# Performance work log

Hardware: AMD Instinct MI355X
Metric: run time of the kernel (lower is better)

Reference implementation:

```python
import jax, jax.numpy as jnp
import numpy as np

B, S, H, DH = 64, 64, 64, 64  # S == H == DH required by the module's (buggy) shape logic
D = H * DH  # d_feature = 4096


def setup_inputs() -> dict:
    key = jax.random.key(0)
    ks = jax.random.split(key, 9)
    sc = 1.0 / np.sqrt(D).astype(np.float32)
    return {
        "x": jax.random.normal(ks[0], (B, S, D), jnp.float32),
        "Wq": jax.random.normal(ks[1], (D, D), jnp.float32) * sc,
        "bq": jax.random.normal(ks[2], (D,), jnp.float32) * 0.01,
        "Wk": jax.random.normal(ks[3], (D, D), jnp.float32) * sc,
        "bk": jax.random.normal(ks[4], (D,), jnp.float32) * 0.01,
        "Wv": jax.random.normal(ks[5], (D, D), jnp.float32) * sc,
        "bv": jax.random.normal(ks[6], (D,), jnp.float32) * 0.01,
        "Wp": jax.random.normal(ks[7], (D, D), jnp.float32) * sc,
        "bp": jax.random.normal(ks[8], (D,), jnp.float32) * 0.01,
    }


def reference(x, Wq, bq, Wk, bk, Wv, bv, Wp, bp):
    b, s, d = x.shape
    # nn.Linear: y = x @ W^T + b
    q = (x @ Wq.T + bq).reshape(b, s, H, DH)  # _split's permute(0,1,2,3) is identity
    k = (x @ Wk.T + bk).reshape(b, s, H, DH)
    v = (x @ Wv.T + bv).reshape(b, s, H, DH)
    # scores over HEAD axis (per token), shape (b, S, H, H); scale by sqrt(d_k)=sqrt(DH)
    scores = jnp.einsum("bshd,bsed->bshe", q, k) / np.sqrt(DH).astype(np.float32)
    attn = jax.nn.softmax(scores, axis=-1)
    # attn @ V^T : out[b,s,i,j] = sum_k attn[b,s,i,k] * v[b,s,j,k]  (needs H == DH)
    vals = jnp.einsum("bsik,bsjk->bsij", attn, v)  # (b, S, H, H)
    # _merge: permute(0,2,1,3) -> (b, H, S, H), view(b, H, S*H); S*H == d_feature
    merged = jnp.transpose(vals, (0, 2, 1, 3)).reshape(b, H, s * H)
    return merged @ Wp.T + bp  # (b, H, d_feature)
```

## Files before the change

### kernel.cpp

```cpp
#include <hip/hip_runtime.h>

typedef __attribute__((ext_vector_type(8))) __bf16 bf16x8;
typedef __attribute__((ext_vector_type(4))) float f32x4;

__device__ __forceinline__ float bf2f(unsigned short u) {
    union { unsigned u; float f; } c; c.u = ((unsigned)u) << 16; return c.f;
}
__device__ __forceinline__ unsigned short f2bf(float f) {
    union { float f; unsigned u; } c; c.f = f;
    unsigned r = c.u + 0x7fffu + ((c.u >> 16) & 1u);
    return (unsigned short)(r >> 16);
}

#define GLD_LDS16(g, l) \
    __builtin_amdgcn_global_load_lds( \
        (const __attribute__((address_space(1))) void*)(g), \
        (__attribute__((address_space(3))) void*)(l), 16, 0, 0)

__global__ void __launch_bounds__(256) cvt_f32_bf16(
    const float* __restrict__ s0, unsigned short* __restrict__ d0,
    const float* __restrict__ s1, unsigned short* __restrict__ d1,
    const float* __restrict__ s2, unsigned short* __restrict__ d2,
    const float* __restrict__ s3, unsigned short* __restrict__ d3,
    const float* __restrict__ s4, unsigned short* __restrict__ d4)
{
    const float* s; unsigned short* d;
    if (blockIdx.z == 0)      { s = s0; d = d0; }
    else if (blockIdx.z == 1) { s = s1; d = d1; }
    else if (blockIdx.z == 2) { s = s2; d = d2; }
    else if (blockIdx.z == 3) { s = s3; d = d3; }
    else                      { s = s4; d = d4; }
    const size_t N = (size_t)4096 * 4096;
    const size_t stride = (size_t)gridDim.x * 256 * 4;
    for (size_t i = ((size_t)blockIdx.x * 256 + threadIdx.x) * 4; i < N; i += stride) {
        float4 v = *(const float4*)(s + i);
        ushort4 o;
        o.x = f2bf(v.x); o.y = f2bf(v.y); o.z = f2bf(v.z); o.w = f2bf(v.w);
        *(ushort4*)(d + i) = o;
    }
}

template <bool OUTF32>
__global__ void __launch_bounds__(512, 2) gemm256(
    const unsigned short* __restrict__ A,
    const unsigned short* __restrict__ W0, const float* __restrict__ b0, void* __restrict__ C0,
    const unsigned short* __restrict__ W1, const float* __restrict__ b1, void* __restrict__ C1,
    const unsigned short* __restrict__ W2, const float* __restrict__ b2, void* __restrict__ C2)
{
    constexpr int K = 4096;
    constexpr int NT = 64;
    extern __shared__ char smem[];

    const unsigned short* W; const float* bias; void* C;
    if (blockIdx.z == 0)      { W = W0; bias = b0; C = C0; }
    else if (blockIdx.z == 1) { W = W1; bias = b1; C = C1; }
    else                      { W = W2; bias = b2; C = C2; }

    const int tid  = threadIdx.x;
    const int lane = tid & 63;
    const int wave = tid >> 6;
    const int wm = wave >> 2;
    const int wn = wave & 3;
    const int m0 = blockIdx.y * 256;
    const int n0 = blockIdx.x * 256;

    const int p = tid << 4;
    const int o = p ^ (((p >> 9) & 1) << 5);
    const int srow = ((o >> 11) << 4) | ((o >> 6) & 15);
    const int scol = (((o >> 10) & 1) << 5) | ((o & 63) >> 1);
    const unsigned short* pA = A + (size_t)(m0 + srow) * K + scol;
    const unsigned short* pB = W + (size_t)(n0 + srow) * K + scol;

    const int fl = lane & 15;
    const int qg = lane >> 4;
    int rdoff = (fl << 6) + (qg << 4);
    rdoff ^= (fl & 8) << 2;
    const int aOffc = (wm << 14) + rdoff;
    const int bOffc = 32768 + ((wn >> 1) << 14) + ((wn & 1) << 13) + rdoff;

    f32x4 acc[8][4];
#pragma unroll
    for (int i = 0; i < 8; i++)
#pragma unroll
        for (int j = 0; j < 4; j++) acc[i][j] = (f32x4){0.f, 0.f, 0.f, 0.f};

    bf16x8 af[4][2], bfr0[2][2], bfr1[2][2];

#define STAGE_A(tt, h, bb) do { \
    GLD_LDS16(pA + (size_t)(tt) * 64 + (size_t)(h) * 524288, \
              smem + (bb) * 65536 + (h) * 16384 + (wave << 10)); \
    GLD_LDS16(pA + (size_t)(tt) * 64 + (size_t)(h) * 524288 + 262144, \
              smem + (bb) * 65536 + (h) * 16384 + 8192 + (wave << 10)); \
} while (0)
#define STAGE_B(tt, h, bb) do { \
    GLD_LDS16(pB + (size_t)(tt) * 64 + (size_t)(h) * 524288, \
              smem + (bb) * 65536 + 32768 + (h) * 16384 + (wave << 10)); \
    GLD_LDS16(pB + (size_t)(tt) * 64 + (size_t)(h) * 524288 + 262144, \
              smem + (bb) * 65536 + 32768 + (h) * 16384 + 8192 + (wave << 10)); \
} while (0)

#define RD_A(mh, bb) do { \
    _Pragma("unroll") for (int it_ = 0; it_ < 4; ++it_) \
    _Pragma("unroll") for (int kk_ = 0; kk_ < 2; ++kk_) \
        af[it_][kk_] = *(const bf16x8*)(smem + (bb) * 65536 + aOffc + (mh) * 8192 + it_ * 2048 + kk_ * 1024); \
} while (0)
#define RD_B(nh, dst, bb) do { \
    _Pragma("unroll") for (int jt_ = 0; jt_ < 2; ++jt_) \
    _Pragma("unroll") for (int kk_ = 0; kk_ < 2; ++kk_) \
        dst[jt_][kk_] = *(const bf16x8*)(smem + (bb) * 65536 + bOffc + (nh) * 4096 + jt_ * 2048 + kk_ * 1024); \
} while (0)

#define MM(mh, nh, bset) do { \
    __builtin_amdgcn_s_setprio(1); \
    _Pragma("unroll") for (int it_ = 0; it_ < 4; ++it_) \
    _Pragma("unroll") for (int jt_ = 0; jt_ < 2; ++jt_) \
    _Pragma("unroll") for (int kk_ = 0; kk_ < 2; ++kk_) \
        acc[(mh) * 4 + it_][(nh) * 2 + jt_] = __builtin_amdgcn_mfma_f32_16x16x32_bf16( \
            af[it_][kk_], bset[jt_][kk_], acc[(mh) * 4 + it_][(nh) * 2 + jt_], 0, 0, 0); \
    __builtin_amdgcn_s_setprio(0); \
} while (0)

#define BAR() __builtin_amdgcn_s_barrier()
#define LGKM0 do { \
    asm volatile("s_waitcnt lgkmcnt(0)" ::: "memory"); \
    __builtin_amdgcn_sched_barrier(0); \
} while (0)

#define TILE(t, bb) do { \
    RD_A(0, bb); RD_B(0, bfr0, bb); \
    if ((t) + 1 < NT) STAGE_A((t) + 1, 0, (bb) ^ 1); \
    BAR(); LGKM0; MM(0, 0, bfr0); BAR(); \
    RD_B(1, bfr1, bb); \
    if ((t) + 1 < NT) STAGE_A((t) + 1, 1, (bb) ^ 1); \
    BAR(); LGKM0; MM(0, 1, bfr1); BAR(); \
    RD_A(1, bb); \
    if ((t) + 2 < NT) STAGE_B((t) + 2, 0, (bb)); \
    BAR(); LGKM0; MM(1, 0, bfr0); BAR(); \
    if ((t) + 2 < NT) STAGE_B((t) + 2, 1, (bb)); \
    BAR(); LGKM0; MM(1, 1, bfr1); \
    if ((t) + 2 < NT) { asm volatile("s_waitcnt vmcnt(4)" ::: "memory"); } \
    else              { asm volatile("s_waitcnt vmcnt(0)" ::: "memory"); } \
    BAR(); \
    __builtin_amdgcn_sched_barrier(0); \
} while (0)

    STAGE_A(0, 0, 0); STAGE_A(0, 1, 0);
    STAGE_B(0, 0, 0); STAGE_B(0, 1, 0);
    STAGE_B(1, 0, 1); STAGE_B(1, 1, 1);
    asm volatile("s_waitcnt vmcnt(4)" ::: "memory");
    BAR();
    __builtin_amdgcn_sched_barrier(0);

    for (int t = 0; t < NT; t += 2) {
        TILE(t, 0);
        TILE(t + 1, 1);
    }

    const int r0 = (lane >> 4) << 2;
#pragma unroll
    for (int j = 0; j < 4; ++j) {
        const int col = n0 + wn * 64 + j * 16 + fl;
        const float bj = bias[col];
#pragma unroll
        for (int i = 0; i < 8; ++i) {
            const int row = m0 + wm * 128 + i * 16 + r0;
#pragma unroll
            for (int r = 0; r < 4; ++r) {
                const float val = acc[i][j][r] + bj;
                if constexpr (OUTF32)
                    ((float*)C)[(size_t)(row + r) * 4096 + col] = val;
                else
                    ((unsigned short*)C)[(size_t)(row + r) * 4096 + col] = f2bf(val);
            }
        }
    }
#undef TILE
#undef LGKM0
#undef BAR
#undef MM
#undef RD_B
#undef RD_A
#undef STAGE_B
#undef STAGE_A
}

__global__ void __launch_bounds__(256) attn_mfma(
    const unsigned short* __restrict__ q, const unsigned short* __restrict__ k,
    const unsigned short* __restrict__ v, unsigned short* __restrict__ merged)
{
    __shared__ __align__(16) unsigned short sP[4][64 * 72];

    const int tid  = threadIdx.x;
    const int wave = tid >> 6;
    const int lane = tid & 63;
    const int token = blockIdx.x * 4 + wave;
    const int b = token >> 6, s = token & 63;
    const size_t base = (size_t)token * 4096;

    const int fl = lane & 15;
    const int qg = lane >> 4;

    f32x4 S[4][4];
#pragma unroll
    for (int i = 0; i < 4; i++)
#pragma unroll
        for (int j = 0; j < 4; j++) S[i][j] = (f32x4){0.f, 0.f, 0.f, 0.f};

#pragma unroll
    for (int ks = 0; ks < 2; ks++) {
        bf16x8 aq[4], bk[4];
#pragma unroll
        for (int t = 0; t < 4; t++) {
            aq[t] = *(const bf16x8*)(q + base + (size_t)(t * 16 + fl) * 64 + ks * 32 + qg * 8);
            bk[t] = *(const bf16x8*)(k + base + (size_t)(t * 16 + fl) * 64 + ks * 32 + qg * 8);
        }
#pragma unroll
        for (int i = 0; i < 4; i++)
#pragma unroll
            for (int j = 0; j < 4; j++)
                S[i][j] = __builtin_amdgcn_mfma_f32_16x16x32_bf16(aq[i], bk[j], S[i][j], 0, 0, 0);
    }

    float mrow[4][4];
#pragma unroll
    for (int i = 0; i < 4; i++)
#pragma unroll
        for (int r = 0; r < 4; r++) {
            float m = S[i][0][r];
            m = fmaxf(m, S[i][1][r]); m = fmaxf(m, S[i][2][r]); m = fmaxf(m, S[i][3][r]);
            mrow[i][r] = m;
        }
#pragma unroll
    for (int off = 1; off <= 8; off <<= 1)
#pragma unroll
        for (int i = 0; i < 4; i++)
#pragma unroll
            for (int r = 0; r < 4; r++)
                mrow[i][r] = fmaxf(mrow[i][r], __shfl_xor(mrow[i][r], off));

    float lrow[4][4];
#pragma unroll
    for (int i = 0; i < 4; i++)
#pragma unroll
        for (int r = 0; r < 4; r++) lrow[i][r] = 0.f;
#pragma unroll
    for (int i = 0; i < 4; i++)
#pragma unroll
        for (int j = 0; j < 4; j++)
#pragma unroll
            for (int r = 0; r < 4; r++) {
                const float p = __expf((S[i][j][r] - mrow[i][r]) * 0.125f);
                S[i][j][r] = p;
                lrow[i][r] += p;
            }
#pragma unroll
    for (int off = 1; off <= 8; off <<= 1)
#pragma unroll
        for (int i = 0; i < 4; i++)
#pragma unroll
            for (int r = 0; r < 4; r++)
                lrow[i][r] += __shfl_xor(lrow[i][r], off);

    unsigned short* myP = &sP[wave][0];
#pragma unroll
    for (int i = 0; i < 4; i++)
#pragma unroll
        for (int r = 0; r < 4; r++) {
            const float inv = 1.f / lrow[i][r];
            const int row = i * 16 + qg * 4 + r;
#pragma unroll
            for (int j = 0; j < 4; j++)
                myP[row * 72 + j * 16 + fl] = f2bf(S[i][j][r] * inv);
        }

    f32x4 O[4][4];
#pragma unroll
    for (int i = 0; i < 4; i++)
#pragma unroll
        for (int j = 0; j < 4; j++) O[i][j] = (f32x4){0.f, 0.f, 0.f, 0.f};

#pragma unroll
    for (int ks = 0; ks < 2; ks++) {
        bf16x8 ap[4], bv[4];
#pragma unroll
        for (int t = 0; t < 4; t++) {
            ap[t] = *(const bf16x8*)(myP + (t * 16 + fl) * 72 + ks * 32 + qg * 8);
            bv[t] = *(const bf16x8*)(v + base + (size_t)(t * 16 + fl) * 64 + ks * 32 + qg * 8);
        }
#pragma unroll
        for (int i = 0; i < 4; i++)
#pragma unroll
            for (int j = 0; j < 4; j++)
                O[i][j] = __builtin_amdgcn_mfma_f32_16x16x32_bf16(ap[i], bv[j], O[i][j], 0, 0, 0);
    }

#pragma unroll
    for (int i = 0; i < 4; i++)
#pragma unroll
        for (int r = 0; r < 4; r++) {
            const size_t rowbase = (size_t)(b * 64 + i * 16 + qg * 4 + r) * 4096 + s * 64;
#pragma unroll
            for (int j = 0; j < 4; j++)
                merged[rowbase + j * 16 + fl] = f2bf(O[i][j][r]);
        }
}

extern "C" void kernel_launch(void* const* d_in, const int* in_sizes, int n_in,
                              void* d_out, int out_size, void* d_ws, size_t ws_size,
                              hipStream_t stream)
{
    const float* x  = (const float*)d_in[0];
    const float* Wq = (const float*)d_in[1];
    const float* bq = (const float*)d_in[2];
    const float* Wk = (const float*)d_in[3];
    const float* bk = (const float*)d_in[4];
    const float* Wv = (const float*)d_in[5];
    const float* bv = (const float*)d_in[6];
    const float* Wp = (const float*)d_in[7];
    const float* bp = (const float*)d_in[8];
    float* out = (float*)d_out;

    const size_t MAT = (size_t)4096 * 4096;
    unsigned short* sw = (unsigned short*)d_ws;
    unsigned short* xb     = sw + 0 * MAT;
    unsigned short* Wqb    = sw + 1 * MAT;
    unsigned short* Wkb    = sw + 2 * MAT;
    unsigned short* Wvb    = sw + 3 * MAT;
    unsigned short* q      = sw + 4 * MAT;
    unsigned short* k      = sw + 5 * MAT;
    unsigned short* v      = sw + 6 * MAT;
    unsigned short* merged = xb;

    const bool slot7 = ws_size >= (size_t)8 * MAT * sizeof(unsigned short);
    unsigned short* Wpb = slot7 ? (sw + 7 * MAT) : Wqb;

    static bool attr_done = false;
    if (!attr_done) {
        hipFuncSetAttribute(reinterpret_cast<const void*>(gemm256<false>),
                            hipFuncAttributeMaxDynamicSharedMemorySize, 131072);
        hipFuncSetAttribute(reinterpret_cast<const void*>(gemm256<true>),
                            hipFuncAttributeMaxDynamicSharedMemorySize, 131072);
        attr_done = true;
    }

    if (slot7) {
        cvt_f32_bf16<<<dim3(2048, 1, 5), 256, 0, stream>>>(
            x, xb, Wq, Wqb, Wk, Wkb, Wv, Wvb, Wp, Wpb);
    } else {
        cvt_f32_bf16<<<dim3(2048, 1, 4), 256, 0, stream>>>(
            x, xb, Wq, Wqb, Wk, Wkb, Wv, Wvb, Wp, Wpb);
    }
    gemm256<false><<<dim3(16, 16, 3), 512, 131072, stream>>>(
        xb, Wqb, bq, q, Wkb, bk, k, Wvb, bv, v);
    if (!slot7) {
        cvt_f32_bf16<<<dim3(2048, 1, 1), 256, 0, stream>>>(
            Wp, Wpb, Wp, Wpb, Wp, Wpb, Wp, Wpb, Wp, Wpb);
    }
    attn_mfma<<<dim3(1024), 256, 0, stream>>>(q, k, v, merged);
    gemm256<true><<<dim3(16, 16, 1), 512, 131072, stream>>>(
        merged, Wpb, bp, out, Wpb, bp, out, Wpb, bp, out);
}
```

Baseline: 806.0 us.

## Double-buffer A fragments and overlap LDS reads with MFMA in GEMM main loop

Restructures the GEMM inner tile schedule to keep two sets of A fragments in registers and prefetch the next tile's first A/B fragments from LDS while the last MFMA block runs. Most per-phase workgroup barriers and lgkmcnt(0) waits are removed, leaving one wait and barrier mid-tile and one after the vmcnt wait. The last two tiles are peeled out of the loop. The aim is to hide LDS read latency behind matrix math and cut barrier stalls, at the cost of more VGPRs per wave and a more delicate reliance on implicit ordering between LDS reads and buffer overwrites.

```diff
diff --git a/kernel.cpp b/kernel.cpp
--- a/kernel.cpp
+++ b/kernel.cpp
@@ -84,7 +84,7 @@
 #pragma unroll
         for (int j = 0; j < 4; j++) acc[i][j] = (f32x4){0.f, 0.f, 0.f, 0.f};
 
-    bf16x8 af[4][2], bfr0[2][2], bfr1[2][2];
+    bf16x8 af0[4][2], af1[4][2], bfr0[2][2], bfr1[2][2];
 
 #define STAGE_A(tt, h, bb) do { \
     GLD_LDS16(pA + (size_t)(tt) * 64 + (size_t)(h) * 524288, \
@@ -99,49 +99,50 @@
               smem + (bb) * 65536 + 32768 + (h) * 16384 + 8192 + (wave << 10)); \
 } while (0)
 
-#define RD_A(mh, bb) do { \
+#define RD_ASET(dst, mh, bb) do { \
     _Pragma("unroll") for (int it_ = 0; it_ < 4; ++it_) \
     _Pragma("unroll") for (int kk_ = 0; kk_ < 2; ++kk_) \
-        af[it_][kk_] = *(const bf16x8*)(smem + (bb) * 65536 + aOffc + (mh) * 8192 + it_ * 2048 + kk_ * 1024); \
-} while (0)
-#define RD_B(nh, dst, bb) do { \
+        dst[it_][kk_] = *(const bf16x8*)(smem + (bb) * 65536 + aOffc + (mh) * 8192 + it_ * 2048 + kk_ * 1024); \
+} while (0)
+#define RD_BSET(dst, nh, bb) do { \
     _Pragma("unroll") for (int jt_ = 0; jt_ < 2; ++jt_) \
     _Pragma("unroll") for (int kk_ = 0; kk_ < 2; ++kk_) \
         dst[jt_][kk_] = *(const bf16x8*)(smem + (bb) * 65536 + bOffc + (nh) * 4096 + jt_ * 2048 + kk_ * 1024); \
 } while (0)
 
-#define MM(mh, nh, bset) do { \
+#define MM(mh, nh, aset, bset) do { \
     __builtin_amdgcn_s_setprio(1); \
     _Pragma("unroll") for (int it_ = 0; it_ < 4; ++it_) \
     _Pragma("unroll") for (int jt_ = 0; jt_ < 2; ++jt_) \
     _Pragma("unroll") for (int kk_ = 0; kk_ < 2; ++kk_) \
         acc[(mh) * 4 + it_][(nh) * 2 + jt_] = __builtin_amdgcn_mfma_f32_16x16x32_bf16( \
-            af[it_][kk_], bset[jt_][kk_], acc[(mh) * 4 + it_][(nh) * 2 + jt_], 0, 0, 0); \
+            aset[it_][kk_], bset[jt_][kk_], acc[(mh) * 4 + it_][(nh) * 2 + jt_], 0, 0, 0); \
     __builtin_amdgcn_s_setprio(0); \
 } while (0)
 
 #define BAR() __builtin_amdgcn_s_barrier()
-#define LGKM0 do { \
+#define FENCE() __builtin_amdgcn_sched_barrier(0)
+
+#define TILE(t, bb) do { \
+    RD_BSET(bfr1, 1, bb); \
+    if ((t) + 1 < NT) STAGE_A((t) + 1, 0, (bb) ^ 1); \
+    FENCE(); \
+    MM(0, 0, af0, bfr0); \
+    RD_ASET(af1, 1, bb); \
+    if ((t) + 1 < NT) STAGE_A((t) + 1, 1, (bb) ^ 1); \
+    FENCE(); \
+    MM(0, 1, af0, bfr1); \
     asm volatile("s_waitcnt lgkmcnt(0)" ::: "memory"); \
-    __builtin_amdgcn_sched_barrier(0); \
-} while (0)
-
-#define TILE(t, bb) do { \
-    RD_A(0, bb); RD_B(0, bfr0, bb); \
-    if ((t) + 1 < NT) STAGE_A((t) + 1, 0, (bb) ^ 1); \
-    BAR(); LGKM0; MM(0, 0, bfr0); BAR(); \
-    RD_B(1, bfr1, bb); \
-    if ((t) + 1 < NT) STAGE_A((t) + 1, 1, (bb) ^ 1); \
-    BAR(); LGKM0; MM(0, 1, bfr1); BAR(); \
-    RD_A(1, bb); \
-    if ((t) + 2 < NT) STAGE_B((t) + 2, 0, (bb)); \
-    BAR(); LGKM0; MM(1, 0, bfr0); BAR(); \
-    if ((t) + 2 < NT) STAGE_B((t) + 2, 1, (bb)); \
-    BAR(); LGKM0; MM(1, 1, bfr1); \
+    BAR(); \
+    FENCE(); \
+    if ((t) + 2 < NT) { STAGE_B((t) + 2, 0, (bb)); STAGE_B((t) + 2, 1, (bb)); } \
+    MM(1, 0, af1, bfr0); \
     if ((t) + 2 < NT) { asm volatile("s_waitcnt vmcnt(4)" ::: "memory"); } \
     else              { asm volatile("s_waitcnt vmcnt(0)" ::: "memory"); } \
     BAR(); \
-    __builtin_amdgcn_sched_barrier(0); \
+    FENCE(); \
+    if ((t) + 1 < NT) { RD_ASET(af0, 0, (bb) ^ 1); RD_BSET(bfr0, 0, (bb) ^ 1); FENCE(); } \
+    MM(1, 1, af1, bfr1); \
 } while (0)
 
     STAGE_A(0, 0, 0); STAGE_A(0, 1, 0);
@@ -149,12 +150,16 @@
     STAGE_B(1, 0, 1); STAGE_B(1, 1, 1);
     asm volatile("s_waitcnt vmcnt(4)" ::: "memory");
     BAR();
-    __builtin_amdgcn_sched_barrier(0);
-
-    for (int t = 0; t < NT; t += 2) {
+    FENCE();
+    RD_ASET(af0, 0, 0); RD_BSET(bfr0, 0, 0);
+    FENCE();
+
+    for (int t = 0; t < 62; t += 2) {
         TILE(t, 0);
         TILE(t + 1, 1);
     }
+    TILE(62, 0);
+    TILE(63, 1);
 
     const int r0 = (lane >> 4) << 2;
 #pragma unroll
@@ -175,11 +180,11 @@
         }
     }
 #undef TILE
-#undef LGKM0
+#undef FENCE
 #undef BAR
 #undef MM
-#undef RD_B
-#undef RD_A
+#undef RD_BSET
+#undef RD_ASET
 #undef STAGE_B
 #undef STAGE_A
 }
```

New measurement: 943.9 us. 1.17x slower.
